# Performance work log

Measured on AMD Instinct MI355X. Metric: run time of the kernel, lower is better.

## Reference

```python
import jax, jax.numpy as jnp
import numpy as np

B, S, D = 4, 2048, 1024
H, Dh = 16, 64


def setup_inputs() -> dict:
    key = jax.random.key(0)
    ks = jax.random.split(key, 9)
    s_in = 1.0 / np.sqrt(D)
    inp = {
        "key": jax.random.normal(ks[0], (B, S, D), jnp.float32),
        "value": jax.random.normal(ks[1], (B, S, D), jnp.float32),
        "query": jax.random.normal(ks[2], (B, S, D), jnp.float32),
        # Linear weights stored as [in, out] (math-equivalent to torch W.T)
        "Wq": jax.random.uniform(ks[3], (D, H * Dh), jnp.float32, -s_in, s_in),
        "bq": jax.random.uniform(ks[4], (H * Dh,), jnp.float32, -s_in, s_in),
        "Wk": jax.random.uniform(ks[5], (D, H * Dh), jnp.float32, -s_in, s_in),
        "bk": jax.random.uniform(ks[6], (H * Dh,), jnp.float32, -s_in, s_in),
        "Wv": jax.random.uniform(ks[7], (D, H * Dh), jnp.float32, -s_in, s_in),
        "bv": jax.random.uniform(ks[8], (H * Dh,), jnp.float32, -s_in, s_in),
    }
    return inp


def reference(key, value, query, Wq, bq, Wk, bk, Wv, bv):
    b, s, _ = key.shape
    # projections -> [B, H, S, Dh]
    q = (query @ Wq + bq).reshape(b, s, H, Dh).transpose(0, 2, 1, 3)
    k = (key @ Wk + bk).reshape(b, s, H, Dh).transpose(0, 2, 1, 3)
    v = (value @ Wv + bv).reshape(b, s, H, Dh).transpose(0, 2, 1, 3)
    scores = jnp.einsum("bhqd,bhkd->bhqk", q, k) / np.sqrt(Dh).astype(np.float32)
    p = jax.nn.softmax(scores, axis=-1)
    out = jnp.einsum("bhqk,bhkd->bhqd", p, v)  # [B, H, S, Dh]
    return out.transpose(0, 2, 1, 3).reshape(b, s, H * Dh)
```

## Files before the change

### kernel.cpp

```cpp
#include <hip/hip_runtime.h>

typedef __bf16 bf16;
typedef __bf16 bf16x8 __attribute__((ext_vector_type(8)));
typedef __bf16 bf16x4 __attribute__((ext_vector_type(4)));
typedef _Float16 f16x4 __attribute__((ext_vector_type(4)));
typedef _Float16 f16x8 __attribute__((ext_vector_type(8)));
typedef float  f32x4  __attribute__((ext_vector_type(4)));

#define LOG2E 1.44269504088896340736f
#define SCQ (0.125f * LOG2E)

__device__ __forceinline__ void async16(const void* g, void* l) {
  __builtin_amdgcn_global_load_lds(
      (const __attribute__((address_space(1))) unsigned int*)g,
      (__attribute__((address_space(3))) unsigned int*)l, 16, 0, 0);
}

__device__ __forceinline__ f32x4 mfma_bf16(bf16x8 a, bf16x8 b, f32x4 c) {
  return __builtin_amdgcn_mfma_f32_16x16x32_bf16(a, b, c, 0, 0, 0);
}
__device__ __forceinline__ f32x4 mfma_f16k16(f16x4 a, f16x4 b, f32x4 c) {
  return __builtin_amdgcn_mfma_f32_16x16x16f16(a, b, c, 0, 0, 0);
}

__global__ __launch_bounds__(256) void prep(const float* __restrict__ q,
                                            const float* __restrict__ k,
                                            const float* __restrict__ v,
                                            const float* __restrict__ W0,
                                            const float* __restrict__ W1,
                                            const float* __restrict__ W2,
                                            bf16* __restrict__ actb,
                                            bf16* __restrict__ Wt) {
  __shared__ float t[64 * 69];
  const int z = blockIdx.y, tid = threadIdx.x;
  if (blockIdx.x < 4096) {
    const float* in = z == 0 ? q : (z == 1 ? k : v);
    bf16* o = actb + (size_t)z * 8388608;
    int i = blockIdx.x * 256 + tid;
    const float4* p = (const float4*)in;
    float4 a = p[i * 2], c = p[i * 2 + 1];
    bf16x8 r;
    r[0] = (bf16)a.x; r[1] = (bf16)a.y; r[2] = (bf16)a.z; r[3] = (bf16)a.w;
    r[4] = (bf16)c.x; r[5] = (bf16)c.y; r[6] = (bf16)c.z; r[7] = (bf16)c.w;
    ((bf16x8*)o)[i] = r;
  } else {
    const float* W = z == 0 ? W0 : (z == 1 ? W1 : W2);
    bf16* O = Wt + (size_t)z * (1024 * 1024);
    int lin = blockIdx.x - 4096;
    int k0 = (lin & 15) * 64, n0 = (lin >> 4) * 64;
    int r0 = tid >> 4, c0 = (tid & 15) * 4;
#pragma unroll
    for (int rr = 0; rr < 4; rr++) {
      int kk = r0 + rr * 16;
      float4 vv = *(const float4*)(W + (k0 + kk) * 1024 + n0 + c0);
      t[kk * 69 + c0 + 0] = vv.x; t[kk * 69 + c0 + 1] = vv.y;
      t[kk * 69 + c0 + 2] = vv.z; t[kk * 69 + c0 + 3] = vv.w;
    }
    __syncthreads();
#pragma unroll
    for (int rr = 0; rr < 4; rr++) {
      int n = r0 + rr * 16;
      bf16x4 o;
#pragma unroll
      for (int j = 0; j < 4; j++) o[j] = (bf16)t[(c0 + j) * 69 + n];
      *(bf16x4*)(O + (n0 + n) * 1024 + k0 + c0) = o;
    }
  }
}

__global__ __launch_bounds__(256, 3) void gemm_qkv(const bf16* __restrict__ Act,
                                                   const bf16* __restrict__ Wt,
                                                   const float* __restrict__ b0,
                                                   const float* __restrict__ b1,
                                                   const float* __restrict__ b2,
                                                   bf16* __restrict__ qo,
                                                   bf16* __restrict__ ko,
                                                   _Float16* __restrict__ vf) {
  __shared__ bf16 smem[16384];
  bf16* sA = smem;
  bf16* sB = smem + 8192;
  const int tid = threadIdx.x;
  const int wave = tid >> 6, lane = tid & 63;
  const int quad = lane >> 4, l15 = lane & 15;
  const int z = blockIdx.z;
  const int m0 = blockIdx.x * 128, n0 = blockIdx.y * 128;
  const bf16* A = Act + (size_t)z * 8388608;
  const bf16* Bt = Wt + (size_t)z * 1048576;
  const float* bias = z == 0 ? b0 : (z == 1 ? b1 : b2);

  const bf16* ap[4]; const bf16* bp[4]; int lo[4];
#pragma unroll
  for (int i = 0; i < 4; i++) {
    int g = wave * 256 + i * 64 + lane;
    int row = g >> 3, jl = (g & 7) ^ (row & 7);
    ap[i] = A + (m0 + row) * 1024 + jl * 8;
    bp[i] = Bt + (n0 + row) * 1024 + jl * 8;
    lo[i] = (wave * 256 + i * 64) * 8;
  }
  const int wm = (wave & 1) * 64, wn = (wave >> 1) * 64;
  f32x4 acc[4][4] = {};

  for (int kt = 0; kt < 16; kt++) {
    const int ko_ = kt * 64;
#pragma unroll
    for (int i = 0; i < 4; i++) async16(ap[i] + ko_, sA + lo[i]);
#pragma unroll
    for (int i = 0; i < 4; i++) async16(bp[i] + ko_, sB + lo[i]);
    __syncthreads();
#pragma unroll
    for (int ks = 0; ks < 2; ks++) {
      bf16x8 af[4], bv[4];
#pragma unroll
      for (int mt = 0; mt < 4; mt++) {
        int m = wm + mt * 16 + l15;
        int ph = (ks * 4 + quad) ^ (m & 7);
        af[mt] = *(const bf16x8*)(sA + m * 64 + ph * 8);
      }
#pragma unroll
      for (int nt = 0; nt < 4; nt++) {
        int n = wn + nt * 16 + l15;
        int ph = (ks * 4 + quad) ^ (n & 7);
        bv[nt] = *(const bf16x8*)(sB + n * 64 + ph * 8);
      }
#pragma unroll
      for (int mt = 0; mt < 4; mt++)
#pragma unroll
        for (int nt = 0; nt < 4; nt++)
          acc[mt][nt] = mfma_bf16(af[mt], bv[nt], acc[mt][nt]);
    }
    __syncthreads();
  }

  if (z != 2) {
    bf16* O = z == 0 ? qo : ko;
    const float sc = z == 0 ? SCQ : 1.0f;
#pragma unroll
    for (int nt = 0; nt < 4; nt++) {
      int n = n0 + wn + nt * 16 + l15;
      float bc = bias[n];
#pragma unroll
      for (int mt = 0; mt < 4; mt++)
#pragma unroll
        for (int r = 0; r < 4; r++) {
          int m = m0 + wm + mt * 16 + quad * 4 + r;
          O[m * 1024 + n] = (bf16)((acc[mt][nt][r] + bc) * sc);
        }
    }
  } else {
    const int b = m0 >> 11, s0 = m0 & 2047;
    const int kvb64 = (s0 + wm) >> 6;
#pragma unroll
    for (int k2 = 0; k2 < 2; k2++) {
      int nn = n0 + wn + k2 * 32;
      int h = nn >> 6, np = (nn >> 5) & 1;
      float bc0 = bias[nn + l15];
      float bc1 = bias[nn + 16 + l15];
#pragma unroll
      for (int mt = 0; mt < 4; mt++) {
        f16x8 pk;
#pragma unroll
        for (int r = 0; r < 4; r++) {
          pk[r]     = (_Float16)(acc[mt][2 * k2][r] + bc0);
          pk[4 + r] = (_Float16)(acc[mt][2 * k2 + 1][r] + bc1);
        }
        size_t off = ((((size_t)(b * 16 + h) * 32 + kvb64) * 8 + (mt * 2 + np)) * 64 + lane) * 8;
        *(f16x8*)(vf + off) = pk;
      }
    }
  }
}

__global__ __launch_bounds__(256, 4) void attn(const bf16* __restrict__ Q,
                                               const bf16* __restrict__ K,
                                               const _Float16* __restrict__ VF,
                                               float* __restrict__ Out) {
  __shared__ bf16 sQ[8192];
  __shared__ bf16 sK[8192];
  __shared__ _Float16 sV[8192];
  const int tid = threadIdx.x;
  const int wave = tid >> 6, lane = tid & 63;
  const int quad = lane >> 4, l15 = lane & 15;
  const int q0 = blockIdx.x * 128, h = blockIdx.y, b = blockIdx.z;
  const bf16* Kbase = K + (size_t)(b * 2048) * 1024 + h * 64;
  const _Float16* Vbase = VF + (size_t)(b * 16 + h) * 131072;

#pragma unroll
  for (int i = 0; i < 4; i++) {
    int g = i * 256 + tid;
    int row = g >> 3, jl = (g & 7) ^ (row & 7);
    async16(Q + (size_t)(b * 2048 + q0 + row) * 1024 + h * 64 + jl * 8, sQ + g * 8);
    async16(Kbase + (size_t)row * 1024 + jl * 8, sK + g * 8);
    async16(Vbase + g * 8, sV + g * 8);
  }
  __syncthreads();

  bf16x8 qf[2][2];
#pragma unroll
  for (int qt2 = 0; qt2 < 2; qt2++)
#pragma unroll
    for (int ks = 0; ks < 2; ks++) {
      int m = wave * 32 + qt2 * 16 + l15;
      int ph = (ks * 4 + quad) ^ (l15 & 7);
      qf[qt2][ks] = *(const bf16x8*)(sQ + m * 64 + ph * 8);
    }

  f32x4 oaccT[2][4] = {};
  float ls[2] = {0.f, 0.f};
  const int ph0 = quad ^ (l15 & 7), ph1 = (4 + quad) ^ (l15 & 7);

  for (int kvb = 0; kvb < 16; kvb++) {
#pragma unroll
    for (int t = 0; t < 8; t++) {
      int row = t * 16 + l15;
      bf16x8 kf0 = *(const bf16x8*)(sK + row * 64 + ph0 * 8);
      bf16x8 kf1 = *(const bf16x8*)(sK + row * 64 + ph1 * 8);
      f32x4 st0 = {}, st1 = {};
      st0 = mfma_bf16(kf0, qf[0][0], st0);
      st0 = mfma_bf16(kf1, qf[0][1], st0);
      st1 = mfma_bf16(kf0, qf[1][0], st1);
      st1 = mfma_bf16(kf1, qf[1][1], st1);
      f16x4 pf0, pf1;
#pragma unroll
      for (int r = 0; r < 4; r++) {
        float p0 = __builtin_amdgcn_exp2f(st0[r]);
        float p1 = __builtin_amdgcn_exp2f(st1[r]);
        ls[0] += p0; ls[1] += p1;
        pf0[r] = (_Float16)p0; pf1[r] = (_Float16)p1;
      }
      const _Float16* sVt = sV + (t >> 2) * 4096 + (t & 3) * 1024;
#pragma unroll
      for (int np = 0; np < 2; np++) {
        f16x8 va2 = *(const f16x8*)(sVt + np * 512 + lane * 8);
        f16x4 lo = __builtin_shufflevector(va2, va2, 0, 1, 2, 3);
        f16x4 hi = __builtin_shufflevector(va2, va2, 4, 5, 6, 7);
        oaccT[0][2 * np]     = mfma_f16k16(lo, pf0, oaccT[0][2 * np]);
        oaccT[0][2 * np + 1] = mfma_f16k16(hi, pf0, oaccT[0][2 * np + 1]);
        oaccT[1][2 * np]     = mfma_f16k16(lo, pf1, oaccT[1][2 * np]);
        oaccT[1][2 * np + 1] = mfma_f16k16(hi, pf1, oaccT[1][2 * np + 1]);
      }
    }
    __syncthreads();
    if (kvb < 15) {
      int kn = (kvb + 1) * 128;
#pragma unroll
      for (int i = 0; i < 4; i++) {
        int g = i * 256 + tid;
        int row = g >> 3, jl = (g & 7) ^ (row & 7);
        async16(Kbase + (size_t)(kn + row) * 1024 + jl * 8, sK + g * 8);
        async16(Vbase + (kvb + 1) * 8192 + g * 8, sV + g * 8);
      }
      __syncthreads();
    }
  }

#pragma unroll
  for (int qt2 = 0; qt2 < 2; qt2++) {
    float l = ls[qt2];
    l += __shfl_xor(l, 16);
    l += __shfl_xor(l, 32);
    float inv = 1.f / l;
    int qrow = b * 2048 + q0 + wave * 32 + qt2 * 16 + l15;
#pragma unroll
    for (int dt = 0; dt < 4; dt++) {
      float4 v;
      v.x = oaccT[qt2][dt][0] * inv;
      v.y = oaccT[qt2][dt][1] * inv;
      v.z = oaccT[qt2][dt][2] * inv;
      v.w = oaccT[qt2][dt][3] * inv;
      *(float4*)(Out + (size_t)qrow * 1024 + h * 64 + dt * 16 + quad * 4) = v;
    }
  }
}

extern "C" void kernel_launch(void* const* d_in, const int* in_sizes, int n_in,
                              void* d_out, int out_size, void* d_ws, size_t ws_size,
                              hipStream_t stream) {
  const float* key   = (const float*)d_in[0];
  const float* value = (const float*)d_in[1];
  const float* query = (const float*)d_in[2];
  const float* Wq = (const float*)d_in[3];
  const float* bq = (const float*)d_in[4];
  const float* Wk = (const float*)d_in[5];
  const float* bk = (const float*)d_in[6];
  const float* Wv = (const float*)d_in[7];
  const float* bv = (const float*)d_in[8];
  float* out = (float*)d_out;

  char* ws = (char*)d_ws;
  bf16* actb   = (bf16*)(ws);
  bf16* wt     = (bf16*)(ws + 50331648);
  bf16* qo     = (bf16*)(ws + 56623104);
  bf16* ko     = (bf16*)(ws + 73400320);
  _Float16* vf = (_Float16*)(ws + 90177536);
  (void)in_sizes; (void)n_in; (void)out_size; (void)ws_size;

  prep<<<dim3(4352, 3), 256, 0, stream>>>(query, key, value, Wq, Wk, Wv, actb, wt);
  gemm_qkv<<<dim3(64, 8, 3), 256, 0, stream>>>(actb, wt, bq, bk, bv, qo, ko, vf);
  attn<<<dim3(16, 16, 4), 256, 0, stream>>>(qo, ko, vf, out);
}
```

Measured before the change: 304.7 us.

## Switch attention to 32x32 MFMA tiles with matching V fragment layout

Rewrites the attention inner loop to use 32x32x16 bf16 MFMA for QK^T and 32x32x8 f16 MFMA for PV instead of 16x16 variants. The V projection epilogue writes a new fragment layout matching the 32x32 operand order. Probabilities are packed with cvt_pkrtz. Larger MFMA tiles cut instruction count and LDS fragment reads per FLOP but raise register pressure, so launch bounds drop occupancy from 4 to 3 blocks per CU.

```diff
diff --git a/kernel.cpp b/kernel.cpp
--- a/kernel.cpp
+++ b/kernel.cpp
@@ -3,9 +3,13 @@
 typedef __bf16 bf16;
 typedef __bf16 bf16x8 __attribute__((ext_vector_type(8)));
 typedef __bf16 bf16x4 __attribute__((ext_vector_type(4)));
+typedef _Float16 f16x2 __attribute__((ext_vector_type(2)));
 typedef _Float16 f16x4 __attribute__((ext_vector_type(4)));
 typedef _Float16 f16x8 __attribute__((ext_vector_type(8)));
+typedef __fp16 h16x2 __attribute__((ext_vector_type(2)));
+typedef __fp16 h16x4 __attribute__((ext_vector_type(4)));
 typedef float  f32x4  __attribute__((ext_vector_type(4)));
+typedef float  f32x16 __attribute__((ext_vector_type(16)));
 
 #define LOG2E 1.44269504088896340736f
 #define SCQ (0.125f * LOG2E)
@@ -19,8 +23,11 @@
 __device__ __forceinline__ f32x4 mfma_bf16(bf16x8 a, bf16x8 b, f32x4 c) {
   return __builtin_amdgcn_mfma_f32_16x16x32_bf16(a, b, c, 0, 0, 0);
 }
-__device__ __forceinline__ f32x4 mfma_f16k16(f16x4 a, f16x4 b, f32x4 c) {
-  return __builtin_amdgcn_mfma_f32_16x16x16f16(a, b, c, 0, 0, 0);
+__device__ __forceinline__ f32x16 mfma32_bf16(bf16x8 a, bf16x8 b, f32x16 c) {
+  return __builtin_amdgcn_mfma_f32_32x32x16_bf16(a, b, c, 0, 0, 0);
+}
+__device__ __forceinline__ f32x16 mfma32x8_f16(f16x4 a, f16x4 b, f32x16 c) {
+  return __builtin_amdgcn_mfma_f32_32x32x8f16(a, b, c, 0, 0, 0);
 }
 
 __global__ __launch_bounds__(256) void prep(const float* __restrict__ q,
@@ -148,29 +155,30 @@
     }
   } else {
     const int b = m0 >> 11, s0 = m0 & 2047;
-    const int kvb64 = (s0 + wm) >> 6;
-#pragma unroll
-    for (int k2 = 0; k2 < 2; k2++) {
-      int nn = n0 + wn + k2 * 32;
-      int h = nn >> 6, np = (nn >> 5) & 1;
-      float bc0 = bias[nn + l15];
-      float bc1 = bias[nn + 16 + l15];
+    const int kvb = s0 >> 7;
+    const int mtg0 = (wave & 1) * 4;
+    const int w = quad >> 1, hl = quad & 1;
+#pragma unroll
+    for (int nt = 0; nt < 4; nt++) {
+      int n = n0 + wn + nt * 16;
+      int hh = n >> 6, db = (n >> 5) & 1;
+      int lanep = hl * 32 + (nt & 1) * 16 + l15;
+      float bc = bias[n + l15];
 #pragma unroll
       for (int mt = 0; mt < 4; mt++) {
-        f16x8 pk;
-#pragma unroll
-        for (int r = 0; r < 4; r++) {
-          pk[r]     = (_Float16)(acc[mt][2 * k2][r] + bc0);
-          pk[4 + r] = (_Float16)(acc[mt][2 * k2 + 1][r] + bc1);
-        }
-        size_t off = ((((size_t)(b * 16 + h) * 32 + kvb64) * 8 + (mt * 2 + np)) * 64 + lane) * 8;
-        *(f16x8*)(vf + off) = pk;
-      }
-    }
-  }
-}
-
-__global__ __launch_bounds__(256, 4) void attn(const bf16* __restrict__ Q,
+        int fi = (mtg0 + mt) * 2 + db;
+        f16x4 pk;
+#pragma unroll
+        for (int r = 0; r < 4; r++) pk[r] = (_Float16)(acc[mt][nt][r] + bc);
+        size_t off = ((((size_t)(b * 16 + hh) * 16 + kvb) * 16 + fi) * 512)
+                     + lanep * 8 + w * 4;
+        *(f16x4*)(vf + off) = pk;
+      }
+    }
+  }
+}
+
+__global__ __launch_bounds__(256, 3) void attn(const bf16* __restrict__ Q,
                                                const bf16* __restrict__ K,
                                                const _Float16* __restrict__ VF,
                                                float* __restrict__ Out) {
@@ -179,65 +187,68 @@
   __shared__ _Float16 sV[8192];
   const int tid = threadIdx.x;
   const int wave = tid >> 6, lane = tid & 63;
-  const int quad = lane >> 4, l15 = lane & 15;
-  const int q0 = blockIdx.x * 128, h = blockIdx.y, b = blockIdx.z;
-  const bf16* Kbase = K + (size_t)(b * 2048) * 1024 + h * 64;
-  const _Float16* Vbase = VF + (size_t)(b * 16 + h) * 131072;
+  const int l31 = lane & 31, hl = lane >> 5;
+  const int q0 = blockIdx.x * 128, hh = blockIdx.y, b = blockIdx.z;
+  const bf16* Kbase = K + (size_t)(b * 2048) * 1024 + hh * 64;
+  const _Float16* Vbase = VF + (size_t)(b * 16 + hh) * 131072;
 
 #pragma unroll
   for (int i = 0; i < 4; i++) {
     int g = i * 256 + tid;
     int row = g >> 3, jl = (g & 7) ^ (row & 7);
-    async16(Q + (size_t)(b * 2048 + q0 + row) * 1024 + h * 64 + jl * 8, sQ + g * 8);
+    async16(Q + (size_t)(b * 2048 + q0 + row) * 1024 + hh * 64 + jl * 8, sQ + g * 8);
     async16(Kbase + (size_t)row * 1024 + jl * 8, sK + g * 8);
     async16(Vbase + g * 8, sV + g * 8);
   }
   __syncthreads();
 
-  bf16x8 qf[2][2];
-#pragma unroll
-  for (int qt2 = 0; qt2 < 2; qt2++)
-#pragma unroll
-    for (int ks = 0; ks < 2; ks++) {
-      int m = wave * 32 + qt2 * 16 + l15;
-      int ph = (ks * 4 + quad) ^ (l15 & 7);
-      qf[qt2][ks] = *(const bf16x8*)(sQ + m * 64 + ph * 8);
-    }
-
-  f32x4 oaccT[2][4] = {};
-  float ls[2] = {0.f, 0.f};
-  const int ph0 = quad ^ (l15 & 7), ph1 = (4 + quad) ^ (l15 & 7);
+  bf16x8 qf[4];
+  {
+    int rowq = wave * 32 + l31, rx = rowq & 7;
+#pragma unroll
+    for (int i = 0; i < 4; i++)
+      qf[i] = *(const bf16x8*)(sQ + rowq * 64 + ((2 * i + hl) ^ rx) * 8);
+  }
+
+  f32x16 oacc[2] = {};
+  float ls = 0.f;
 
   for (int kvb = 0; kvb < 16; kvb++) {
 #pragma unroll
-    for (int t = 0; t < 8; t++) {
-      int row = t * 16 + l15;
-      bf16x8 kf0 = *(const bf16x8*)(sK + row * 64 + ph0 * 8);
-      bf16x8 kf1 = *(const bf16x8*)(sK + row * 64 + ph1 * 8);
-      f32x4 st0 = {}, st1 = {};
-      st0 = mfma_bf16(kf0, qf[0][0], st0);
-      st0 = mfma_bf16(kf1, qf[0][1], st0);
-      st1 = mfma_bf16(kf0, qf[1][0], st1);
-      st1 = mfma_bf16(kf1, qf[1][1], st1);
-      f16x4 pf0, pf1;
-#pragma unroll
-      for (int r = 0; r < 4; r++) {
-        float p0 = __builtin_amdgcn_exp2f(st0[r]);
-        float p1 = __builtin_amdgcn_exp2f(st1[r]);
-        ls[0] += p0; ls[1] += p1;
-        pf0[r] = (_Float16)p0; pf1[r] = (_Float16)p1;
-      }
-      const _Float16* sVt = sV + (t >> 2) * 4096 + (t & 3) * 1024;
-#pragma unroll
-      for (int np = 0; np < 2; np++) {
-        f16x8 va2 = *(const f16x8*)(sVt + np * 512 + lane * 8);
-        f16x4 lo = __builtin_shufflevector(va2, va2, 0, 1, 2, 3);
-        f16x4 hi = __builtin_shufflevector(va2, va2, 4, 5, 6, 7);
-        oaccT[0][2 * np]     = mfma_f16k16(lo, pf0, oaccT[0][2 * np]);
-        oaccT[0][2 * np + 1] = mfma_f16k16(hi, pf0, oaccT[0][2 * np + 1]);
-        oaccT[1][2 * np]     = mfma_f16k16(lo, pf1, oaccT[1][2 * np]);
-        oaccT[1][2 * np + 1] = mfma_f16k16(hi, pf1, oaccT[1][2 * np + 1]);
-      }
+    for (int t32 = 0; t32 < 4; t32++) {
+      int rowk = t32 * 32 + l31, rx = rowk & 7;
+      const bf16* kr = sK + rowk * 64;
+      f32x16 st = {};
+#pragma unroll
+      for (int i = 0; i < 4; i++) {
+        bf16x8 kf = *(const bf16x8*)(kr + ((2 * i + hl) ^ rx) * 8);
+        st = mfma32_bf16(kf, qf[i], st);
+      }
+      f16x4 pf[4];
+      float ps = 0.f;
+#pragma unroll
+      for (int s = 0; s < 4; s++) {
+        float p0 = __builtin_amdgcn_exp2f(st[4 * s + 0]);
+        float p1 = __builtin_amdgcn_exp2f(st[4 * s + 1]);
+        float p2 = __builtin_amdgcn_exp2f(st[4 * s + 2]);
+        float p3 = __builtin_amdgcn_exp2f(st[4 * s + 3]);
+        ps += (p0 + p1) + (p2 + p3);
+        h16x2 c0 = __builtin_amdgcn_cvt_pkrtz(p0, p1);
+        h16x2 c1 = __builtin_amdgcn_cvt_pkrtz(p2, p3);
+        h16x4 cc = __builtin_shufflevector(c0, c1, 0, 1, 2, 3);
+        pf[s] = __builtin_bit_cast(f16x4, cc);
+      }
+      ls += ps;
+#pragma unroll
+      for (int u = 0; u < 2; u++)
+#pragma unroll
+        for (int db = 0; db < 2; db++) {
+          f16x8 va2 = *(const f16x8*)(sV + ((t32 * 4 + u * 2 + db) * 64 + lane) * 8);
+          f16x4 vlo = __builtin_shufflevector(va2, va2, 0, 1, 2, 3);
+          f16x4 vhi = __builtin_shufflevector(va2, va2, 4, 5, 6, 7);
+          oacc[db] = mfma32x8_f16(vlo, pf[2 * u], oacc[db]);
+          oacc[db] = mfma32x8_f16(vhi, pf[2 * u + 1], oacc[db]);
+        }
     }
     __syncthreads();
     if (kvb < 15) {
@@ -253,23 +264,21 @@
     }
   }
 
-#pragma unroll
-  for (int qt2 = 0; qt2 < 2; qt2++) {
-    float l = ls[qt2];
-    l += __shfl_xor(l, 16);
-    l += __shfl_xor(l, 32);
-    float inv = 1.f / l;
-    int qrow = b * 2048 + q0 + wave * 32 + qt2 * 16 + l15;
-#pragma unroll
-    for (int dt = 0; dt < 4; dt++) {
+  ls += __shfl_xor(ls, 32);
+  float inv = 1.f / ls;
+  int qrow = b * 2048 + q0 + wave * 32 + l31;
+  float* orow = Out + (size_t)qrow * 1024 + hh * 64;
+#pragma unroll
+  for (int db = 0; db < 2; db++)
+#pragma unroll
+    for (int rg = 0; rg < 4; rg++) {
       float4 v;
-      v.x = oaccT[qt2][dt][0] * inv;
-      v.y = oaccT[qt2][dt][1] * inv;
-      v.z = oaccT[qt2][dt][2] * inv;
-      v.w = oaccT[qt2][dt][3] * inv;
-      *(float4*)(Out + (size_t)qrow * 1024 + h * 64 + dt * 16 + quad * 4) = v;
-    }
-  }
+      v.x = oacc[db][4 * rg + 0] * inv;
+      v.y = oacc[db][4 * rg + 1] * inv;
+      v.z = oacc[db][4 * rg + 2] * inv;
+      v.w = oacc[db][4 * rg + 3] * inv;
+      *(float4*)(orow + db * 32 + rg * 8 + 4 * hl) = v;
+    }
 }
 
 extern "C" void kernel_launch(void* const* d_in, const int* in_sizes, int n_in,
```

After: 302.0 us. About the same (-0.9%).
